# Kernel optimization log

Measured on AMD Instinct MI355X. Metric: run time of the kernel, lower is better.

Reference implementation:

```python
import jax, jax.numpy as jnp
import numpy as np

N_NODES = 50000
N_EDGES = 800000
H = 128
T = 2


def setup_inputs() -> dict:
    key = jax.random.key(0)
    ks = jax.random.split(key, 8)
    s = 0.05
    return {
        "h": jax.random.normal(ks[0], (N_NODES, H), jnp.float32),
        "edges": jax.random.randint(ks[1], (N_EDGES, 2), 0, N_NODES, jnp.int64),
        "W_msg": jax.random.normal(ks[2], (T, 2 * H, 2 * H), jnp.float32) * s,
        "b_msg": jax.random.normal(ks[3], (T, 2 * H), jnp.float32) * s,
        "W_ih": jax.random.normal(ks[4], (T, 3 * H, 2 * H), jnp.float32) * s,
        "W_hh": jax.random.normal(ks[5], (T, 3 * H, H), jnp.float32) * s,
        "b_ih": jax.random.normal(ks[6], (T, 3 * H), jnp.float32) * s,
        "b_hh": jax.random.normal(ks[7], (T, 3 * H), jnp.float32) * s,
    }


def reference(h, edges, W_msg, b_msg, W_ih, W_hh, b_ih, b_hh):
    n_nodes, hd = h.shape
    src, dst = edges[:, 0], edges[:, 1]
    # nodes with at least one incoming edge get GRU-updated; others keep state
    deg = jax.ops.segment_sum(jnp.ones(edges.shape[0], h.dtype), dst,
                              num_segments=n_nodes)
    has_msg = (deg > 0)[:, None]
    for t in range(W_msg.shape[0]):
        # per-edge message: Linear(cat(h_src, h_dst))  [E, 2H]
        m_in = jnp.concatenate([h[src], h[dst]], axis=-1)
        m = m_in @ W_msg[t].T + b_msg[t]
        # scatter-sum messages into destination nodes  [N, 2H]
        agg = jax.ops.segment_sum(m, dst, num_segments=n_nodes)
        # GRUCell(agg, h)
        gi = agg @ W_ih[t].T + b_ih[t]   # [N, 3H]
        gh = h @ W_hh[t].T + b_hh[t]     # [N, 3H]
        ir, iz, inn = gi[:, :hd], gi[:, hd:2 * hd], gi[:, 2 * hd:]
        hr, hz, hn = gh[:, :hd], gh[:, hd:2 * hd], gh[:, 2 * hd:]
        r = jax.nn.sigmoid(ir + hr)
        z = jax.nn.sigmoid(iz + hz)
        n = jnp.tanh(inn + r * hn)
        h_new = (1.0 - z) * n + z * h
        h = jnp.where(has_msg, h_new, h)
    return h
```

## Files before the change

kernel.cpp:

```cpp
#include <hip/hip_runtime.h>
#include <hip/hip_bf16.h>

#define NN 50000
#define NE 800000
#define HD 128
#define G3 384
#define K2 256
#define NTILES 3125
#define S8 16
#define DENSE 64

typedef short s16x8 __attribute__((ext_vector_type(8)));
typedef float f32x4 __attribute__((ext_vector_type(4)));

static __device__ __forceinline__ ushort f2b(float f) {
    __hip_bfloat16 b = __float2bfloat16(f);
    return *(ushort*)&b;
}
static __device__ __forceinline__ float b2f(ushort u) {
    return __uint_as_float(((uint)u) << 16);
}
static __device__ __forceinline__ uint pk(ushort a, ushort b) {
    return (uint)a | ((uint)b << 16);
}
static __device__ __forceinline__ float fsig(float x) {
    return __builtin_amdgcn_rcpf(1.f + __builtin_amdgcn_exp2f(-x * 1.44269504f));
}
static __device__ __forceinline__ float ftanh(float x) {
    return 1.f - 2.f * __builtin_amdgcn_rcpf(1.f + __builtin_amdgcn_exp2f(x * 2.88539008f));
}

static __device__ __forceinline__ void gl_lds16(const void* g, void* l) {
    __builtin_amdgcn_global_load_lds(
        (const __attribute__((address_space(1))) uint*)(uintptr_t)g,
        (__attribute__((address_space(3))) uint*)(uintptr_t)l, 16, 0, 0);
}

__global__ void k_fill1(const int* __restrict__ edges, int* __restrict__ cnt8,
                        ushort* __restrict__ slots8, uint* __restrict__ ovf,
                        int* __restrict__ ovfc) {
    int e = blockIdx.x * blockDim.x + threadIdx.x;
    if (e >= NE) return;
    int reg = blockIdx.x & 7;
    int s = edges[2 * e];
    int d = edges[2 * e + 1];
    int pos = atomicAdd(&cnt8[reg * NN + d], 1);
    if (pos < S8) {
        slots8[((size_t)reg * NN + d) * S8 + pos] = (ushort)s;
    } else {
        int o = atomicAdd(ovfc, 1);
        ovf[o] = ((uint)d << 16) | (uint)s;
    }
}

__global__ void k_merge(const int* __restrict__ cnt8, const ushort* __restrict__ slots8,
                        ushort* __restrict__ dense, int* __restrict__ deg_tot,
                        int* __restrict__ dcnt, uint* __restrict__ ovf,
                        int* __restrict__ ovfc) {
    int v = blockIdx.x * blockDim.x + threadIdx.x;
    if (v >= NN) return;
    int dg = 0, pos = 0;
    ushort* dst = dense + (size_t)v * DENSE;
#pragma unroll
    for (int r = 0; r < 8; r++) {
        int c = cnt8[r * NN + v];
        dg += c;
        int cc = c < S8 ? c : S8;
        const ushort* src = slots8 + ((size_t)r * NN + v) * S8;
        for (int j = 0; j < cc; j++) {
            ushort s = src[j];
            if (pos < DENSE) {
                dst[pos] = s;
            } else {
                int o = atomicAdd(ovfc, 1);
                ovf[o] = ((uint)v << 16) | (uint)s;
            }
            pos++;
        }
    }
    deg_tot[v] = dg;
    dcnt[v] = pos < DENSE ? pos : DENSE;
}

__global__ void k_pre0(const float* __restrict__ W_ih, const float* __restrict__ W_msg,
                       const float* __restrict__ b_msg, const float* __restrict__ h,
                       float* __restrict__ B1, float* __restrict__ c3,
                       ushort* __restrict__ hb) {
    int b = blockIdx.x;
    int tid = threadIdx.x;
    if (b < 768) {
        int idx = b * 256 + tid;
        int k = idx % K2;
        int n = (idx / K2) % G3;
        int t = idx / (K2 * G3);
        const float* wi = W_ih + ((size_t)t * G3 + n) * K2;
        const float* wm = W_msg + (size_t)t * K2 * K2;
        float acc = 0.f;
#pragma unroll 8
        for (int j = 0; j < K2; j++) acc += wi[j] * wm[(size_t)j * K2 + k];
        B1[((size_t)t * K2 + k) * G3 + n] = acc;
    } else if (b < 771) {
        int idx = (b - 768) * 256 + tid;
        if (idx >= 2 * G3) return;
        int n = idx % G3;
        int t = idx / G3;
        const float* wi = W_ih + ((size_t)t * G3 + n) * K2;
        const float* bm = b_msg + t * K2;
        float acc = 0.f;
#pragma unroll 8
        for (int j = 0; j < K2; j++) acc += wi[j] * bm[j];
        c3[idx] = acc;
    } else {
        int i = (b - 771) * 256 + tid;
        if (i >= NN * HD / 4) return;
        float4 v = reinterpret_cast<const float4*>(h)[i];
        ushort4 o;
        o.x = f2b(v.x); o.y = f2b(v.y); o.z = f2b(v.z); o.w = f2b(v.w);
        reinterpret_cast<ushort4*>(hb)[i] = o;
    }
}

__global__ void k_pre1(const float* __restrict__ B1, const float* __restrict__ W_hh,
                       const float* __restrict__ b_ih, const float* __restrict__ b_hh,
                       const float* __restrict__ c3, ushort* __restrict__ Bq,
                       float* __restrict__ bih_p, float* __restrict__ bhh_p,
                       float* __restrict__ c3_p) {
    int b = blockIdx.x;
    int tid = threadIdx.x;
    if (b < 192) {
        int idx = b * 256 + tid;
        int lane = idx & 63;
        int slot = (idx >> 6) % 48;
        int slice = ((idx >> 6) / 48) % 8;
        int t = idx / (64 * 48 * 8);
        int slab = slot / 12;
        int rem = slot % 12;
        int kb = rem / 3, gate = rem % 3;
        int d = slice * 16 + (lane & 15);
        int kbase = kb * 32 + (lane >> 4) * 8;
        ushort* dst = Bq + (size_t)idx * 8;
#pragma unroll
        for (int e = 0; e < 8; e++) {
            int k = kbase + e;
            float v;
            if (slab == 0) {
                v = B1[((size_t)t * K2 + k) * G3 + gate * 128 + d];
            } else if (slab == 3) {
                v = W_hh[((size_t)t * G3 + gate * 128 + d) * HD + k];
            } else {
                float full = B1[((size_t)t * K2 + 128 + k) * G3 + gate * 128 + d];
                v = (slab == 1) ? full : (full - b2f(f2b(full)));
            }
            dst[e] = f2b(v);
        }
    } else {
        int idx = (b - 192) * 256 + tid;
        if (idx >= 2 * 8 * 3 * 16) return;
        int c = idx & 15;
        int g = (idx >> 4) % 3;
        int slice = ((idx >> 4) / 3) % 8;
        int t = idx / (16 * 3 * 8);
        int d = slice * 16 + c;
        bih_p[idx] = b_ih[t * G3 + g * 128 + d];
        bhh_p[idx] = b_hh[t * G3 + g * 128 + d];
        c3_p[idx]  = c3[t * G3 + g * 128 + d];
    }
}

__global__ void k_prep(const ushort* __restrict__ hb, const float* __restrict__ hf,
                       const int* __restrict__ deg_tot, const int* __restrict__ dcnt,
                       const ushort* __restrict__ dense,
                       const uint* __restrict__ ovf, const int* __restrict__ ovfc,
                       ushort* __restrict__ FA) {
    int wv = (blockIdx.x * blockDim.x + threadIdx.x) >> 6;
    int lane = threadIdx.x & 63;
    if (wv >= NN) return;
    int dg = deg_tot[wv];
    int lim = dcnt[wv];
    const ushort* sl = dense + (size_t)wv * DENSE;
    float a0 = 0.f, a1 = 0.f;
    int j = 0;
    for (; j + 16 <= lim; j += 16) {
        uint v[16];
#pragma unroll
        for (int q = 0; q < 16; q++) {
            int s = sl[j + q];
            v[q] = *reinterpret_cast<const uint*>(hb + (size_t)s * HD + lane * 2);
        }
#pragma unroll
        for (int q = 0; q < 16; q++) {
            a0 += b2f((ushort)(v[q] & 0xffff));
            a1 += b2f((ushort)(v[q] >> 16));
        }
    }
    for (; j + 4 <= lim; j += 4) {
        uint v[4];
#pragma unroll
        for (int q = 0; q < 4; q++) {
            int s = sl[j + q];
            v[q] = *reinterpret_cast<const uint*>(hb + (size_t)s * HD + lane * 2);
        }
#pragma unroll
        for (int q = 0; q < 4; q++) {
            a0 += b2f((ushort)(v[q] & 0xffff));
            a1 += b2f((ushort)(v[q] >> 16));
        }
    }
    for (; j < lim; j++) {
        int s = sl[j];
        uint v = *reinterpret_cast<const uint*>(hb + (size_t)s * HD + lane * 2);
        a0 += b2f((ushort)(v & 0xffff));
        a1 += b2f((ushort)(v >> 16));
    }
    if (dg > lim) {
        int oc = *ovfc;
        for (int k = 0; k < oc; k++) {
            uint pr = ovf[k];
            if ((int)(pr >> 16) == wv) {
                int s = (int)(pr & 0xffffu);
                uint v = *reinterpret_cast<const uint*>(hb + (size_t)s * HD + lane * 2);
                a0 += b2f((ushort)(v & 0xffff));
                a1 += b2f((ushort)(v >> 16));
            }
        }
    }
    int tile = wv >> 4, r = wv & 15;
    int kb = lane >> 4;
    int lp = r + (((lane & 15) >> 2) << 4);
    uint* base = reinterpret_cast<uint*>(FA) + (size_t)tile * 4096 + kb * 256 +
                 lp * 4 + (lane & 3);
    float2 hv = *reinterpret_cast<const float2*>(hf + (size_t)wv * HD + lane * 2);
    float dgf = (float)dg;
    float dh0 = dgf * hv.x, dh1 = dgf * hv.y;
    ushort p0 = f2b(dh0), p1 = f2b(dh1);
    ushort l0 = f2b(dh0 - b2f(p0)), l1 = f2b(dh1 - b2f(p1));
    base[0]    = pk(f2b(a0), f2b(a1));
    base[1024] = pk(p0, p1);
    base[2048] = pk(l0, l1);
    base[3072] = pk(f2b(hv.x), f2b(hv.y));
}

#define BS(slab, kb, nf) \
    (*reinterpret_cast<const s16x8*>(&Bs[(size_t)((((slab) * 12 + (kb) * 3 + (nf)) * 64 + lane)) * 8]))

__global__ __launch_bounds__(512) void k_fused(
    const ushort* __restrict__ FA,
    const ushort* __restrict__ Bq_t,
    const float* __restrict__ bih_t,
    const float* __restrict__ bhh_t,
    const float* __restrict__ c3_t,
    const int* __restrict__ deg,
    const float* __restrict__ hcur,
    float* __restrict__ hout,
    ushort* __restrict__ hb_out)
{
    __shared__ __align__(16) ushort Bs[48 * 512];

    int tid = threadIdx.x;
    int bid = blockIdx.x;
    int r8 = bid & 7;
    int q = bid >> 3;
    int oct = (q >> 3) * 8 + r8;
    int slice = q & 7;
    if (oct * 32 >= NTILES) return;
    int w = tid >> 6;
    int lane = tid & 63;
    int lhi = lane >> 4;
    int col = lane & 15;

    const ushort* Bg = Bq_t + (size_t)slice * 48 * 512;
#pragma unroll
    for (int i = 0; i < 6; i++) {
        int seg = w * 6 + i;
        gl_lds16(Bg + (size_t)seg * 512 + lane * 8, &Bs[(size_t)seg * 512]);
    }

    int d = (slice << 4) + col;
    float bihv[3], bhhv[3], c3v[3];
#pragma unroll
    for (int g = 0; g < 3; g++) {
        int o = (slice * 3 + g) * 16 + col;
        bihv[g] = bih_t[o];
        bhhv[g] = bhh_t[o];
        c3v[g] = c3_t[o];
    }

    __syncthreads();

#pragma unroll
    for (int it = 0; it < 4; it++) {
        int t = oct * 32 + w + 8 * it;
        if (t >= NTILES) break;
        const ushort* FAt = FA + (size_t)t * 8192;

        s16x8 As[4], Ahh[4], Ahl[4], Ah[4];
#pragma unroll
        for (int kb = 0; kb < 4; kb++) {
            As[kb]  = *reinterpret_cast<const s16x8*>(FAt + ((size_t)(kb) * 64 + lane) * 8);
            Ahh[kb] = *reinterpret_cast<const s16x8*>(FAt + ((size_t)(4 + kb) * 64 + lane) * 8);
            Ahl[kb] = *reinterpret_cast<const s16x8*>(FAt + ((size_t)(8 + kb) * 64 + lane) * 8);
            Ah[kb]  = *reinterpret_cast<const s16x8*>(FAt + ((size_t)(12 + kb) * 64 + lane) * 8);
        }

        int rbase0 = t * 16 + (lhi << 2);
        float hv[4];
        int dgi[4];
#pragma unroll
        for (int r = 0; r < 4; r++) {
            int m = rbase0 + r;
            int mm = m < NN ? m : 0;
            hv[r] = hcur[(size_t)mm * HD + d];
            dgi[r] = deg[mm];
        }

        f32x4 accI[3], accH[3];
#pragma unroll
        for (int i = 0; i < 3; i++) {
            accI[i] = f32x4{0.f, 0.f, 0.f, 0.f};
            accH[i] = f32x4{0.f, 0.f, 0.f, 0.f};
        }

#pragma unroll
        for (int kb = 0; kb < 4; kb++) {
#pragma unroll
            for (int nf = 0; nf < 3; nf++) {
                s16x8 b0 = BS(0, kb, nf);
                accI[nf] = __builtin_amdgcn_mfma_f32_16x16x32_bf16(As[kb], b0, accI[nf], 0, 0, 0);
                s16x8 b1 = BS(1, kb, nf);
                accI[nf] = __builtin_amdgcn_mfma_f32_16x16x32_bf16(Ahh[kb], b1, accI[nf], 0, 0, 0);
                accI[nf] = __builtin_amdgcn_mfma_f32_16x16x32_bf16(Ahl[kb], b1, accI[nf], 0, 0, 0);
                s16x8 b2 = BS(2, kb, nf);
                accI[nf] = __builtin_amdgcn_mfma_f32_16x16x32_bf16(Ahh[kb], b2, accI[nf], 0, 0, 0);
                s16x8 b3 = BS(3, kb, nf);
                accH[nf] = __builtin_amdgcn_mfma_f32_16x16x32_bf16(Ah[kb], b3, accH[nf], 0, 0, 0);
            }
        }

#pragma unroll
        for (int r = 0; r < 4; r++) {
            int m = rbase0 + r;
            bool wr = m < NN;
            float dgf = (float)dgi[r];
            float ir  = accI[0][r] + dgf * c3v[0] + bihv[0];
            float iz  = accI[1][r] + dgf * c3v[1] + bihv[1];
            float in_ = accI[2][r] + dgf * c3v[2] + bihv[2];
            float hr = accH[0][r] + bhhv[0];
            float hz = accH[1][r] + bhhv[1];
            float hn = accH[2][r] + bhhv[2];
            float rg = fsig(ir + hr);
            float zg = fsig(iz + hz);
            float ng = ftanh(in_ + rg * hn);
            float hnew = (1.f - zg) * ng + zg * hv[r];
            float res = (dgi[r] > 0) ? hnew : hv[r];
            if (wr) {
                hout[(size_t)m * HD + d] = res;
                hb_out[(size_t)m * HD + d] = f2b(res);
            }
        }
    }
}

extern "C" void kernel_launch(void* const* d_in, const int* in_sizes, int n_in,
                              void* d_out, int out_size, void* d_ws, size_t ws_size,
                              hipStream_t stream) {
    const float* h_in  = (const float*)d_in[0];
    const int*   edges = (const int*)d_in[1];
    const float* W_msg = (const float*)d_in[2];
    const float* b_msg = (const float*)d_in[3];
    const float* W_ih  = (const float*)d_in[4];
    const float* W_hh  = (const float*)d_in[5];
    const float* b_ih  = (const float*)d_in[6];
    const float* b_hh  = (const float*)d_in[7];
    float* out = (float*)d_out;

    char* p = (char*)d_ws;
    auto alloc = [&](size_t bytes) {
        void* r = (void*)p;
        p += (bytes + 255) / 256 * 256;
        return r;
    };
    int*    cnt8    = (int*)alloc((size_t)(8 * NN + 1) * 4);
    ushort* slots8  = (ushort*)alloc((size_t)8 * NN * S8 * 2);
    ushort* dense   = (ushort*)alloc((size_t)NN * DENSE * 2);
    uint*   ovf     = (uint*)alloc((size_t)NE * 4);
    int*    deg_tot = (int*)alloc((size_t)NN * 4);
    int*    dcnt    = (int*)alloc((size_t)NN * 4);
    float*  B1      = (float*)alloc((size_t)2 * K2 * G3 * 4);
    float*  c3      = (float*)alloc((size_t)2 * G3 * 4);
    ushort* Bq      = (ushort*)alloc((size_t)2 * 8 * 48 * 512 * 2);
    float*  bih_p   = (float*)alloc((size_t)2 * 8 * 3 * 16 * 4);
    float*  bhh_p   = (float*)alloc((size_t)2 * 8 * 3 * 16 * 4);
    float*  c3_p    = (float*)alloc((size_t)2 * 8 * 3 * 16 * 4);
    ushort* hb0     = (ushort*)alloc((size_t)NN * HD * 2);
    ushort* hb1     = (ushort*)alloc((size_t)NN * HD * 2);
    ushort* FA      = (ushort*)alloc((size_t)NTILES * 8192 * 2);
    float*  h1      = (float*)alloc((size_t)NN * HD * 4);
    int*    ovfc    = cnt8 + 8 * NN;

    hipMemsetAsync(cnt8, 0, (size_t)(8 * NN + 1) * 4, stream);
    k_fill1<<<(NE + 255) / 256, 256, 0, stream>>>(edges, cnt8, slots8, ovf, ovfc);
    k_merge<<<(NN + 255) / 256, 256, 0, stream>>>(cnt8, slots8, dense, deg_tot, dcnt,
                                                  ovf, ovfc);
    k_pre0<<<771 + (NN * HD / 4 + 255) / 256, 256, 0, stream>>>(
        W_ih, W_msg, b_msg, h_in, B1, c3, hb0);
    k_pre1<<<195, 256, 0, stream>>>(B1, W_hh, b_ih, b_hh, c3, Bq, bih_p, bhh_p, c3_p);

    const int FGRID = 832;
    const size_t BqT = (size_t)8 * 48 * 512;
    const size_t biasT = (size_t)8 * 3 * 16;

    k_prep<<<(NN * 64 + 255) / 256, 256, 0, stream>>>(hb0, h_in, deg_tot, dcnt, dense,
                                                      ovf, ovfc, FA);
    k_fused<<<FGRID, 512, 0, stream>>>(FA, Bq, bih_p, bhh_p, c3_p, deg_tot, h_in, h1, hb1);
    k_prep<<<(NN * 64 + 255) / 256, 256, 0, stream>>>(hb1, h1, deg_tot, dcnt, dense,
                                                      ovf, ovfc, FA);
    k_fused<<<FGRID, 512, 0, stream>>>(FA, Bq + BqT, bih_p + biasT, bhh_p + biasT,
                                       c3_p + biasT, deg_tot, h1, out, hb0);
}
```

Baseline: 262.8 us.

## Build deg*h split-bf16 and h A-operands inside fused kernel instead of staging in FA

```diff
diff --git a/kernel.cpp b/kernel.cpp
--- a/kernel.cpp
+++ b/kernel.cpp
@@ -22,6 +22,11 @@
 }
 static __device__ __forceinline__ uint pk(ushort a, ushort b) {
     return (uint)a | ((uint)b << 16);
+}
+static __device__ __forceinline__ s16x8 mk8(uint a, uint b, uint c, uint d) {
+    union { uint4 u; s16x8 v; } x;
+    x.u = uint4{a, b, c, d};
+    return x.v;
 }
 static __device__ __forceinline__ float fsig(float x) {
     return __builtin_amdgcn_rcpf(1.f + __builtin_amdgcn_exp2f(-x * 1.44269504f));
@@ -167,7 +172,7 @@
     }
 }
 
-__global__ void k_prep(const ushort* __restrict__ hb, const float* __restrict__ hf,
+__global__ void k_prep(const ushort* __restrict__ hb,
                        const int* __restrict__ deg_tot, const int* __restrict__ dcnt,
                        const ushort* __restrict__ dense,
                        const uint* __restrict__ ovf, const int* __restrict__ ovfc,
@@ -227,17 +232,8 @@
     int tile = wv >> 4, r = wv & 15;
     int kb = lane >> 4;
     int lp = r + (((lane & 15) >> 2) << 4);
-    uint* base = reinterpret_cast<uint*>(FA) + (size_t)tile * 4096 + kb * 256 +
-                 lp * 4 + (lane & 3);
-    float2 hv = *reinterpret_cast<const float2*>(hf + (size_t)wv * HD + lane * 2);
-    float dgf = (float)dg;
-    float dh0 = dgf * hv.x, dh1 = dgf * hv.y;
-    ushort p0 = f2b(dh0), p1 = f2b(dh1);
-    ushort l0 = f2b(dh0 - b2f(p0)), l1 = f2b(dh1 - b2f(p1));
-    base[0]    = pk(f2b(a0), f2b(a1));
-    base[1024] = pk(p0, p1);
-    base[2048] = pk(l0, l1);
-    base[3072] = pk(f2b(hv.x), f2b(hv.y));
+    reinterpret_cast<uint*>(FA)[(size_t)tile * 1024 + kb * 256 + lp * 4 + (lane & 3)] =
+        pk(f2b(a0), f2b(a1));
 }
 
 #define BS(slab, kb, nf) \
@@ -251,6 +247,7 @@
     const float* __restrict__ c3_t,
     const int* __restrict__ deg,
     const float* __restrict__ hcur,
+    const ushort* __restrict__ hb_in,
     float* __restrict__ hout,
     ushort* __restrict__ hb_out)
 {
@@ -291,16 +288,12 @@
     for (int it = 0; it < 4; it++) {
         int t = oct * 32 + w + 8 * it;
         if (t >= NTILES) break;
-        const ushort* FAt = FA + (size_t)t * 8192;
-
-        s16x8 As[4], Ahh[4], Ahl[4], Ah[4];
-#pragma unroll
-        for (int kb = 0; kb < 4; kb++) {
-            As[kb]  = *reinterpret_cast<const s16x8*>(FAt + ((size_t)(kb) * 64 + lane) * 8);
-            Ahh[kb] = *reinterpret_cast<const s16x8*>(FAt + ((size_t)(4 + kb) * 64 + lane) * 8);
-            Ahl[kb] = *reinterpret_cast<const s16x8*>(FAt + ((size_t)(8 + kb) * 64 + lane) * 8);
-            Ah[kb]  = *reinterpret_cast<const s16x8*>(FAt + ((size_t)(12 + kb) * 64 + lane) * 8);
-        }
+        const ushort* FAt = FA + (size_t)t * 2048;
+        int arow = t * 16 + col;
+        float dgfa = (float)deg[arow];
+        const float*  hfr = hcur + (size_t)arow * HD;
+        const ushort* hbr = hb_in + (size_t)arow * HD;
+        int koff = lhi * 8;
 
         int rbase0 = t * 16 + (lhi << 2);
         float hv[4];
@@ -308,9 +301,8 @@
 #pragma unroll
         for (int r = 0; r < 4; r++) {
             int m = rbase0 + r;
-            int mm = m < NN ? m : 0;
-            hv[r] = hcur[(size_t)mm * HD + d];
-            dgi[r] = deg[mm];
+            hv[r] = hcur[(size_t)m * HD + d];
+            dgi[r] = deg[m];
         }
 
         f32x4 accI[3], accH[3];
@@ -322,24 +314,42 @@
 
 #pragma unroll
         for (int kb = 0; kb < 4; kb++) {
+            s16x8 As = *reinterpret_cast<const s16x8*>(FAt + ((size_t)(kb * 64 + lane)) * 8);
+            s16x8 Ah = *reinterpret_cast<const s16x8*>(hbr + kb * 32 + koff);
+            float hfv[8];
+            *reinterpret_cast<float4*>(&hfv[0]) =
+                *reinterpret_cast<const float4*>(hfr + kb * 32 + koff);
+            *reinterpret_cast<float4*>(&hfv[4]) =
+                *reinterpret_cast<const float4*>(hfr + kb * 32 + koff + 4);
+            ushort hi[8], lo[8];
+#pragma unroll
+            for (int e = 0; e < 8; e++) {
+                float dh = dgfa * hfv[e];
+                ushort pp = f2b(dh);
+                hi[e] = pp;
+                lo[e] = f2b(dh - b2f(pp));
+            }
+            s16x8 Ahh = mk8(pk(hi[0], hi[1]), pk(hi[2], hi[3]),
+                            pk(hi[4], hi[5]), pk(hi[6], hi[7]));
+            s16x8 Ahl = mk8(pk(lo[0], lo[1]), pk(lo[2], lo[3]),
+                            pk(lo[4], lo[5]), pk(lo[6], lo[7]));
 #pragma unroll
             for (int nf = 0; nf < 3; nf++) {
                 s16x8 b0 = BS(0, kb, nf);
-                accI[nf] = __builtin_amdgcn_mfma_f32_16x16x32_bf16(As[kb], b0, accI[nf], 0, 0, 0);
+                accI[nf] = __builtin_amdgcn_mfma_f32_16x16x32_bf16(As, b0, accI[nf], 0, 0, 0);
                 s16x8 b1 = BS(1, kb, nf);
-                accI[nf] = __builtin_amdgcn_mfma_f32_16x16x32_bf16(Ahh[kb], b1, accI[nf], 0, 0, 0);
-                accI[nf] = __builtin_amdgcn_mfma_f32_16x16x32_bf16(Ahl[kb], b1, accI[nf], 0, 0, 0);
+                accI[nf] = __builtin_amdgcn_mfma_f32_16x16x32_bf16(Ahh, b1, accI[nf], 0, 0, 0);
+                accI[nf] = __builtin_amdgcn_mfma_f32_16x16x32_bf16(Ahl, b1, accI[nf], 0, 0, 0);
                 s16x8 b2 = BS(2, kb, nf);
-                accI[nf] = __builtin_amdgcn_mfma_f32_16x16x32_bf16(Ahh[kb], b2, accI[nf], 0, 0, 0);
+                accI[nf] = __builtin_amdgcn_mfma_f32_16x16x32_bf16(Ahh, b2, accI[nf], 0, 0, 0);
                 s16x8 b3 = BS(3, kb, nf);
-                accH[nf] = __builtin_amdgcn_mfma_f32_16x16x32_bf16(Ah[kb], b3, accH[nf], 0, 0, 0);
+                accH[nf] = __builtin_amdgcn_mfma_f32_16x16x32_bf16(Ah, b3, accH[nf], 0, 0, 0);
             }
         }
 
 #pragma unroll
         for (int r = 0; r < 4; r++) {
             int m = rbase0 + r;
-            bool wr = m < NN;
             float dgf = (float)dgi[r];
             float ir  = accI[0][r] + dgf * c3v[0] + bihv[0];
             float iz  = accI[1][r] + dgf * c3v[1] + bihv[1];
@@ -352,10 +362,8 @@
             float ng = ftanh(in_ + rg * hn);
             float hnew = (1.f - zg) * ng + zg * hv[r];
             float res = (dgi[r] > 0) ? hnew : hv[r];
-            if (wr) {
-                hout[(size_t)m * HD + d] = res;
-                hb_out[(size_t)m * HD + d] = f2b(res);
-            }
+            hout[(size_t)m * HD + d] = res;
+            hb_out[(size_t)m * HD + d] = f2b(res);
         }
     }
 }
@@ -393,7 +401,7 @@
     float*  c3_p    = (float*)alloc((size_t)2 * 8 * 3 * 16 * 4);
     ushort* hb0     = (ushort*)alloc((size_t)NN * HD * 2);
     ushort* hb1     = (ushort*)alloc((size_t)NN * HD * 2);
-    ushort* FA      = (ushort*)alloc((size_t)NTILES * 8192 * 2);
+    ushort* FA      = (ushort*)alloc((size_t)NTILES * 2048 * 2);
     float*  h1      = (float*)alloc((size_t)NN * HD * 4);
     int*    ovfc    = cnt8 + 8 * NN;
 
@@ -409,11 +417,12 @@
     const size_t BqT = (size_t)8 * 48 * 512;
     const size_t biasT = (size_t)8 * 3 * 16;
 
-    k_prep<<<(NN * 64 + 255) / 256, 256, 0, stream>>>(hb0, h_in, deg_tot, dcnt, dense,
+    k_prep<<<(NN * 64 + 255) / 256, 256, 0, stream>>>(hb0, deg_tot, dcnt, dense,
                                                       ovf, ovfc, FA);
-    k_fused<<<FGRID, 512, 0, stream>>>(FA, Bq, bih_p, bhh_p, c3_p, deg_tot, h_in, h1, hb1);
-    k_prep<<<(NN * 64 + 255) / 256, 256, 0, stream>>>(hb1, h1, deg_tot, dcnt, dense,
+    k_fused<<<FGRID, 512, 0, stream>>>(FA, Bq, bih_p, bhh_p, c3_p, deg_tot,
+                                       h_in, hb0, h1, hb1);
+    k_prep<<<(NN * 64 + 255) / 256, 256, 0, stream>>>(hb1, deg_tot, dcnt, dense,
                                                       ovf, ovfc, FA);
     k_fused<<<FGRID, 512, 0, stream>>>(FA, Bq + BqT, bih_p + biasT, bhh_p + biasT,
-                                       c3_p + biasT, deg_tot, h1, out, hb0);
-}
+                                       c3_p + biasT, deg_tot, h1, hb1, out, hb0);
+}
```

New measurement: 269.9 us. 2.7% more time.
